# Optimization experiments

Hardware: AMD Instinct MI355X
Metric: run time of the kernel (lower is better)

Reference implementation:

```python
import jax, jax.numpy as jnp
import numpy as np

GRID = 2
SPAN = 2.0
EMBED = 64
HIDDEN = 128
PRED_LEN = 12
N = 1024
T = 8
SCENE_SIZE = 64


def _social_pool(ht, pos, scene, active):
    """ht: [N,H], pos: [N,2], scene: [N] int, active: [N] bool -> [N, GRID*GRID, H].
    Vectorized equivalent of the per-scene scatter_add pooling: pairwise mask over
    same-scene, active, within-area, non-self pairs; bin neighbor hidden states."""
    n = ht.shape[0]
    half = SPAN / 2.0
    eps = 0.01
    rel = pos[None, :, :] - pos[:, None, :]  # rel[i,j] = pos_j - pos_i
    within = ((rel[..., 0] < half - eps) & (rel[..., 0] > -half + eps)
              & (rel[..., 1] < half - eps) & (rel[..., 1] > -half + eps))
    pair = (within & (~jnp.eye(n, dtype=bool))
            & (scene[:, None] == scene[None, :])
            & active[:, None] & active[None, :])
    cell = SPAN / GRID
    gidx = jnp.floor((rel + half) / cell).astype(jnp.int32)
    gid = jnp.clip(gidx[..., 0] * GRID + gidx[..., 1], 0, GRID * GRID - 1)
    onehot = jax.nn.one_hot(gid, GRID * GRID, dtype=ht.dtype) * pair[..., None].astype(ht.dtype)
    # pooled[i,g,h] = sum_j onehot[i,j,g] * ht[j,h]
    return jnp.einsum('ijg,jh->igh', onehot, ht)


def _lstm_step(x, h, c, Wih, Whh, bih, bhh):
    z = x @ Wih.T + bih + h @ Whh.T + bhh
    i, f, g, o = jnp.split(z, 4, axis=-1)
    c_new = jax.nn.sigmoid(f) * c + jax.nn.sigmoid(i) * jnp.tanh(g)
    h_new = jax.nn.sigmoid(o) * jnp.tanh(c_new)
    return h_new, c_new


def setup_inputs() -> dict:
    key = jax.random.key(0)
    ks = jax.random.split(key, 16)
    past_traj = jax.random.uniform(ks[0], (N, T, 2), dtype=jnp.float32) * 8.0
    past_traj_rel = jax.random.normal(ks[1], (N, T, 2), dtype=jnp.float32)
    past_traj_timestamp_mask = jnp.ones((N, T), dtype=jnp.int32)
    is_predictable = jnp.ones((N, 1), dtype=jnp.int32)
    same_scene_mask = (jnp.arange(N, dtype=jnp.int32) // SCENE_SIZE).reshape(N, 1)

    def lin(k, fan_out, fan_in):
        b = 1.0 / np.sqrt(fan_in)
        return jax.random.uniform(k, (fan_out, fan_in), jnp.float32, -b, b)

    pos_W = lin(ks[2], EMBED, 2)
    pos_b = jnp.zeros((EMBED,), jnp.float32)
    soc_W = lin(ks[3], EMBED, GRID * GRID * HIDDEN)
    soc_b = jnp.zeros((EMBED,), jnp.float32)
    Wih = lin(ks[4], 4 * HIDDEN, 2 * EMBED)
    Whh = lin(ks[5], 4 * HIDDEN, HIDDEN)
    bih = jnp.zeros((4 * HIDDEN,), jnp.float32)
    bhh = jnp.zeros((4 * HIDDEN,), jnp.float32)
    h0 = jax.random.normal(ks[6], (HIDDEN,), jnp.float32) * 0.1
    c0 = jax.random.normal(ks[7], (HIDDEN,), jnp.float32) * 0.1
    pred_W = lin(ks[8], 5, HIDDEN)
    pred_b = jnp.zeros((5,), jnp.float32)
    return {
        'past_traj': past_traj, 'past_traj_rel': past_traj_rel,
        'past_traj_timestamp_mask': past_traj_timestamp_mask,
        'is_predictable': is_predictable, 'same_scene_mask': same_scene_mask,
        'pos_W': pos_W, 'pos_b': pos_b, 'soc_W': soc_W, 'soc_b': soc_b,
        'Wih': Wih, 'Whh': Whh, 'bih': bih, 'bhh': bhh,
        'h0': h0, 'c0': c0, 'pred_W': pred_W, 'pred_b': pred_b,
    }


def reference(past_traj, past_traj_rel, past_traj_timestamp_mask, is_predictable,
              same_scene_mask, pos_W, pos_b, soc_W, soc_b, Wih, Whh, bih, bhh,
              h0, c0, pred_W, pred_b):
    n = past_traj.shape[0]
    scene = same_scene_mask[:, 0]
    ht = jnp.broadcast_to(h0[None, :], (n, HIDDEN))
    ct = jnp.broadcast_to(c0[None, :], (n, HIDDEN))

    def obs_step(carry, inp):
        ht, ct = carry
        point, rel, m = inp  # [N,2], [N,2], [N]
        active = m == 1
        pooled = _social_pool(ht, point, scene, active)  # [N,G^2,H]
        et = jax.nn.relu(rel @ pos_W.T + pos_b)
        at = jax.nn.relu(pooled.reshape(n, -1) @ soc_W.T + soc_b)
        x = jnp.concatenate([et, at], axis=-1)
        h_new, c_new = _lstm_step(x, ht, ct, Wih, Whh, bih, bhh)
        ht = jnp.where(active[:, None], h_new, ht)
        ct = jnp.where(active[:, None], c_new, ct)
        return (ht, ct), None

    obs_inp = (jnp.moveaxis(past_traj, 1, 0), jnp.moveaxis(past_traj_rel, 1, 0),
               jnp.moveaxis(past_traj_timestamp_mask, 1, 0))
    (ht, ct), _ = jax.lax.scan(obs_step, (ht, ct), obs_inp)

    pred_active = past_traj_timestamp_mask[:, -1] == 1
    pos0 = past_traj[:, -1, :]

    def pred_step(carry, _):
        ht, ct, pos = carry
        out = ht @ pred_W.T + pred_b  # [N,5]
        rel = out[:, :2]
        pos = pos + rel
        pooled = _social_pool(ht, pos, scene, pred_active)
        et = jax.nn.relu(rel @ pos_W.T + pos_b)
        at = jax.nn.relu(pooled.reshape(n, -1) @ soc_W.T + soc_b)
        x = jnp.concatenate([et, at], axis=-1)
        h_new, c_new = _lstm_step(x, ht, ct, Wih, Whh, bih, bhh)
        ht = jnp.where(pred_active[:, None], h_new, ht)
        ct = jnp.where(pred_active[:, None], c_new, ct)
        return (ht, ct, pos), (out, pos)

    (_, _, _), (outs, trajs) = jax.lax.scan(pred_step, (ht, ct, pos0), None, length=PRED_LEN)
    pred_out_all = jnp.where(pred_active[:, None, None], jnp.moveaxis(outs, 0, 1), 0.0)
    pred_traj_all = jnp.where(pred_active[:, None, None], jnp.moveaxis(trajs, 0, 1), 0.0)
    # is_predictable is all-ones in this setup, so the final boolean filter is identity
    return pred_out_all, pred_traj_all
```

## Files before the change

### kernel.cpp

```cpp
#include <hip/hip_runtime.h>

#define NAGENT 64
#define HID    128
#define TOBS   8
#define PREDL  12
#define NTHR   1024
#define XH     136
#define PP     264
#define SPP    268

typedef __attribute__((ext_vector_type(8))) short bf16x8;
typedef __attribute__((ext_vector_type(4))) short bf16x4;
typedef __attribute__((ext_vector_type(4))) float f32x4;
typedef __attribute__((ext_vector_type(2))) unsigned int u32x2;

__device__ __forceinline__ unsigned short f2bf(float f) {
    unsigned int x = __float_as_uint(f);
    unsigned int r = (x + 0x7fffu + ((x >> 16) & 1u)) >> 16;
    return (unsigned short)r;
}
__device__ __forceinline__ float bf2f(unsigned short u) {
    return __uint_as_float(((unsigned int)u) << 16);
}
__device__ __forceinline__ float sigmf(float x) {
    return __builtin_amdgcn_rcpf(1.0f + __expf(-x));
}
__device__ __forceinline__ float tanhf_fast(float x) {
    x = fminf(fmaxf(x, -15.0f), 15.0f);
    float e = __expf(2.0f * x);
    return (e - 1.0f) * __builtin_amdgcn_rcpf(e + 1.0f);
}
__device__ __forceinline__ float sel4(float a0, float a1, float a2, float a3, int k) {
    float lo = (k & 1) ? a1 : a0;
    float hi = (k & 1) ? a3 : a2;
    return (k & 2) ? hi : lo;
}

__global__ void prep_weights(const float* __restrict__ Wih, const float* __restrict__ Whh,
                             const float* __restrict__ socW, const float* __restrict__ predW,
                             unsigned short* __restrict__ wd, unsigned short* __restrict__ wb,
                             unsigned short* __restrict__ wp) {
    int idx = blockIdx.x * 256 + threadIdx.x;
    if (idx < 131072) {
        int e = idx & 7, l = (idx >> 3) & 63, t = idx >> 9;
        int kt = t & 7, nt = t >> 3;
        int k = kt * 32 + ((l >> 4) << 3) + e;
        int n = nt * 16 + (l & 15);
        int d = n >> 2, g = n & 3;
        int row = g * 128 + d;
        float v = (k < 128) ? Wih[row * 128 + k] : Whh[row * 128 + (k - 128)];
        wd[idx] = f2bf(v);
    } else if (idx < 163840) {
        int i2 = idx - 131072;
        int e = i2 & 7, l = (i2 >> 3) & 63, t = i2 >> 9;
        int kt = t & 3, nt = t >> 2;
        int k = kt * 32 + ((l >> 4) << 3) + e;
        int r = nt * 16 + (l & 15);
        int eo = r >> 2, g = r & 3;
        wb[i2] = f2bf(socW[eo * 512 + g * 128 + k]);
    } else if (idx < 167936) {
        int i3 = idx - 163840;
        int e = i3 & 7, l = (i3 >> 3) & 63, f = i3 >> 9;
        int kt = f & 3, half = f >> 2;
        int k = kt * 32 + ((l >> 4) << 3) + e;
        int n = l & 15;
        float v = (n < 5) ? predW[n * 128 + k] : 0.0f;
        unsigned short hi = f2bf(v);
        wp[i3] = half ? f2bf(v - bf2f(hi)) : hi;
    }
}

__global__ __launch_bounds__(NTHR) void social_lstm_mfma(
    const float* __restrict__ past_traj, const float* __restrict__ past_traj_rel,
    const int* __restrict__ ts_mask, const int* __restrict__ scene_in,
    const float* __restrict__ pos_W, const float* __restrict__ pos_b,
    const float* __restrict__ soc_b,
    const float* __restrict__ bih, const float* __restrict__ bhh,
    const float* __restrict__ h0, const float* __restrict__ c0,
    const float* __restrict__ pred_b,
    const unsigned short* __restrict__ wd, const unsigned short* __restrict__ wb,
    const unsigned short* __restrict__ wp,
    float* __restrict__ out)
{
    __shared__ __align__(16) unsigned short sh_X[NAGENT][XH];
    __shared__ __align__(16) unsigned short sh_H[2][NAGENT][XH];
    __shared__ __align__(16) unsigned short sh_P[NAGENT][PP];
    __shared__ __align__(16) unsigned short sh_S[NAGENT][SPP];
    __shared__ float sh_px[2][NAGENT], sh_py[2][NAGENT];
    __shared__ float sh_rx[2][NAGENT], sh_ry[2][NAGENT];
    __shared__ __align__(16) int sh_act[2][NAGENT];
    __shared__ int sh_scene[NAGENT];

    const int tid  = threadIdx.x;
    const int lane = tid & 63;
    const int wv   = __builtin_amdgcn_readfirstlane(tid >> 6);
    const int gbase = blockIdx.x * NAGENT;
    const int c16 = lane & 15;
    const int q4  = lane >> 4;
    const int go  = c16 & 3;
    const int dq  = c16 >> 2;

    float bs[2], c_st[4][2], h_rg[4][2];
    int dimv[2];
    #pragma unroll
    for (int s = 0; s < 2; ++s) {
        const int n = (2 * wv + s) * 16 + c16;
        const int d = n >> 2, g = n & 3;
        bs[s] = bih[g * 128 + d] + bhh[g * 128 + d];
        dimv[s] = (2 * wv + s) * 4 + dq;
        const float hz = h0[dimv[s]], cz = c0[dimv[s]];
        #pragma unroll
        for (int mj = 0; mj < 4; ++mj) { c_st[mj][s] = cz; h_rg[mj][s] = hz; }
    }
    for (int p = tid; p < NAGENT * HID; p += NTHR) {
        int a = p >> 7, d = p & 127;
        sh_H[0][a][d] = f2bf(h0[d]);
    }
    if (tid < NAGENT) {
        const int ig = gbase + tid;
        sh_scene[tid] = scene_in[ig];
        sh_px[0][tid] = past_traj[(ig * TOBS + 0) * 2 + 0];
        sh_py[0][tid] = past_traj[(ig * TOBS + 0) * 2 + 1];
        sh_rx[0][tid] = past_traj_rel[(ig * TOBS + 0) * 2 + 0];
        sh_ry[0][tid] = past_traj_rel[(ig * TOBS + 0) * 2 + 1];
        sh_act[0][tid] = (ts_mask[ig * TOBS + 0] == 1) ? 1 : 0;
    }
    __syncthreads();

    const bf16x8* wdp = (const bf16x8*)wd + (2 * wv * 8) * 64 + lane;
    const bf16x8* wbv = (const bf16x8*)wb;

    for (int step = 0; step < TOBS + PREDL; ++step) {
        const int pb = step & 1;
        const int hb = step & 1;
        const int ab = (step < TOBS) ? pb : 1;

        if (step >= TOBS) {
            if (wv < 4) {
                const bf16x8* wpv = (const bf16x8*)wp;
                f32x4 pa = (f32x4){0.f, 0.f, 0.f, 0.f};
                #pragma unroll
                for (int kt = 0; kt < 4; ++kt) {
                    const bf16x8 a = *(const bf16x8*)&sh_H[hb][wv * 16 + c16][kt * 32 + q4 * 8];
                    pa = __builtin_amdgcn_mfma_f32_16x16x32_bf16(a, wpv[kt * 64 + lane], pa, 0, 0, 0);
                    pa = __builtin_amdgcn_mfma_f32_16x16x32_bf16(a, wpv[(4 + kt) * 64 + lane], pa, 0, 0, 0);
                }
                if (c16 < 5) {
                    const float pbias = pred_b[c16];
                    const int p = step - TOBS;
                    const int pprev = (step - 1) & 1;
                    #pragma unroll
                    for (int rr = 0; rr < 4; ++rr) {
                        const int a = wv * 16 + q4 * 4 + rr;
                        const float o = pa[rr] + pbias;
                        const float m = sh_act[1][a] ? 1.0f : 0.0f;
                        const int ig = gbase + a;
                        out[(ig * PREDL + p) * 5 + c16] = m * o;
                        if (c16 == 0) {
                            const float px = sh_px[pprev][a] + o;
                            sh_px[pb][a] = px; sh_rx[pb][a] = o;
                            out[61440 + (ig * PREDL + p) * 2 + 0] = m * px;
                        }
                        if (c16 == 1) {
                            const float py = sh_py[pprev][a] + o;
                            sh_py[pb][a] = py; sh_ry[pb][a] = o;
                            out[61440 + (ig * PREDL + p) * 2 + 1] = m * py;
                        }
                    }
                }
            } else {
                #pragma unroll
                for (int pass = 0; pass < 2; ++pass) {
                    const int tt = (pass == 0) ? (wv - 4) : (wv + 8);
                    if (pass == 1 && wv >= 8) break;
                    f32x4 acc2[4];
                    #pragma unroll
                    for (int mj = 0; mj < 4; ++mj) acc2[mj] = (f32x4){0.f, 0.f, 0.f, 0.f};
                    #pragma unroll
                    for (int kt = 0; kt < 4; ++kt) {
                        const bf16x8 b = wbv[(tt * 4 + kt) * 64 + lane];
                        #pragma unroll
                        for (int mj = 0; mj < 4; ++mj) {
                            const bf16x8 a = *(const bf16x8*)&sh_H[hb][mj * 16 + c16][kt * 32 + q4 * 8];
                            acc2[mj] = __builtin_amdgcn_mfma_f32_16x16x32_bf16(a, b, acc2[mj], 0, 0, 0);
                        }
                    }
                    const int rcol = tt * 16 + c16;
                    #pragma unroll
                    for (int mj = 0; mj < 4; ++mj)
                        #pragma unroll
                        for (int rr = 0; rr < 4; ++rr)
                            sh_S[mj * 16 + q4 * 4 + rr][rcol] = f2bf(acc2[mj][rr]);
                }
            }
            __syncthreads();
        }

        #pragma unroll
        for (int it = 0; it < 4; ++it) {
            const int p = it * NTHR + tid;
            const int i = p >> 6, j = p & 63;
            const float dx = sh_px[pb][j] - sh_px[pb][i];
            const float dy = sh_py[pb][j] - sh_py[pb][i];
            const bool within = (dx < 0.99f) & (dx > -0.99f) & (dy < 0.99f) & (dy > -0.99f);
            const bool pair = within && (i != j) && (sh_scene[i] == sh_scene[j])
                              && sh_act[ab][i] && sh_act[ab][j];
            const int gid = ((dx >= 0.f) ? 2 : 0) + ((dy >= 0.f) ? 1 : 0);
            unsigned int w0 = 0, w1 = 0;
            if (pair) {
                if (gid == 0) w0 = 0x3f80u;
                else if (gid == 1) w0 = 0x3f800000u;
                else if (gid == 2) w1 = 0x3f80u;
                else w1 = 0x3f800000u;
            }
            u32x2 w; w[0] = w0; w[1] = w1;
            *(u32x2*)&sh_P[i][j * 4] = w;
        }
        {
            const float rx = sh_rx[pb][lane], ry = sh_ry[pb][lane];
            const int e0 = wv * 4;
            #pragma unroll
            for (int u = 0; u < 4; ++u) {
                const int e = e0 + u;
                sh_X[lane][e] = f2bf(fmaxf(pos_b[e] + rx * pos_W[e * 2] + ry * pos_W[e * 2 + 1], 0.f));
            }
        }
        if (step < TOBS) {
            f32x4 acc2[4];
            #pragma unroll
            for (int mj = 0; mj < 4; ++mj) acc2[mj] = (f32x4){0.f, 0.f, 0.f, 0.f};
            #pragma unroll
            for (int kt = 0; kt < 4; ++kt) {
                const bf16x8 b = wbv[(wv * 4 + kt) * 64 + lane];
                #pragma unroll
                for (int mj = 0; mj < 4; ++mj) {
                    const bf16x8 a = *(const bf16x8*)&sh_H[hb][mj * 16 + c16][kt * 32 + q4 * 8];
                    acc2[mj] = __builtin_amdgcn_mfma_f32_16x16x32_bf16(a, b, acc2[mj], 0, 0, 0);
                }
            }
            const int rcol = wv * 16 + c16;
            #pragma unroll
            for (int mj = 0; mj < 4; ++mj)
                #pragma unroll
                for (int rr = 0; rr < 4; ++rr)
                    sh_S[mj * 16 + q4 * 4 + rr][rcol] = f2bf(acc2[mj][rr]);
        }
        __syncthreads();

        {
            const int mt = wv & 3, nt = wv >> 2;
            const int cb = 4 * (nt * 16 + c16);
            f32x4 cac = (f32x4){0.f, 0.f, 0.f, 0.f};
            #pragma unroll
            for (int kt = 0; kt < 8; ++kt) {
                const bf16x8 a = *(const bf16x8*)&sh_P[mt * 16 + c16][kt * 32 + q4 * 8];
                const int j0 = kt * 8 + q4 * 2;
                const bf16x4 lo = *(const bf16x4*)&sh_S[j0][cb];
                const bf16x4 hi = *(const bf16x4*)&sh_S[j0 + 1][cb];
                const bf16x8 b = __builtin_shufflevector(lo, hi, 0, 1, 2, 3, 4, 5, 6, 7);
                cac = __builtin_amdgcn_mfma_f32_16x16x32_bf16(a, b, cac, 0, 0, 0);
            }
            const int e = nt * 16 + c16;
            const float sb = soc_b[e];
            #pragma unroll
            for (int rr = 0; rr < 4; ++rr)
                sh_X[mt * 16 + q4 * 4 + rr][64 + e] = f2bf(fmaxf(cac[rr] + sb, 0.f));
        }
        __syncthreads();

        {
            f32x4 acc[4][2];
            #pragma unroll
            for (int mj = 0; mj < 4; ++mj) {
                acc[mj][0] = (f32x4){0.f, 0.f, 0.f, 0.f};
                acc[mj][1] = (f32x4){0.f, 0.f, 0.f, 0.f};
            }
            #pragma unroll 2
            for (int kt = 0; kt < 8; ++kt) {
                const bf16x8 b0 = wdp[kt * 64];
                const bf16x8 b1 = wdp[kt * 64 + 512];
                #pragma unroll
                for (int mj = 0; mj < 4; ++mj) {
                    const bf16x8 a = (kt < 4)
                        ? *(const bf16x8*)&sh_X[mj * 16 + c16][kt * 32 + q4 * 8]
                        : *(const bf16x8*)&sh_H[hb][mj * 16 + c16][(kt - 4) * 32 + q4 * 8];
                    acc[mj][0] = __builtin_amdgcn_mfma_f32_16x16x32_bf16(a, b0, acc[mj][0], 0, 0, 0);
                    acc[mj][1] = __builtin_amdgcn_mfma_f32_16x16x32_bf16(a, b1, acc[mj][1], 0, 0, 0);
                }
            }
            #pragma unroll
            for (int mj = 0; mj < 4; ++mj) {
                const int a = mj * 16 + q4 * 4 + go;
                const bool act = sh_act[ab][a] != 0;
                #pragma unroll
                for (int s = 0; s < 2; ++s) {
                    const float z0 = acc[mj][s][0] + bs[s];
                    const float z1 = acc[mj][s][1] + bs[s];
                    const float z2 = acc[mj][s][2] + bs[s];
                    const float z3 = acc[mj][s][3] + bs[s];
                    const float s0 = sel4(z0, z1, z2, z3, go);
                    const float s1 = sel4(z0, z1, z2, z3, go ^ 1);
                    const float s2 = sel4(z0, z1, z2, z3, go ^ 2);
                    const float s3 = sel4(z0, z1, z2, z3, go ^ 3);
                    const float t1 = __shfl_xor(s1, 1, 64);
                    const float t2 = __shfl_xor(s2, 2, 64);
                    const float t3 = __shfl_xor(s3, 3, 64);
                    const float zi = sel4(s0, t1, t2, t3, go);
                    const float zf = sel4(s0, t1, t2, t3, go ^ 1);
                    const float zg = sel4(s0, t1, t2, t3, go ^ 2);
                    const float zo = sel4(s0, t1, t2, t3, go ^ 3);
                    const float cold = c_st[mj][s];
                    const float cn = sigmf(zf) * cold + sigmf(zi) * tanhf_fast(zg);
                    const float hn = sigmf(zo) * tanhf_fast(cn);
                    c_st[mj][s] = act ? cn : cold;
                    h_rg[mj][s] = act ? hn : h_rg[mj][s];
                    sh_H[hb ^ 1][a][dimv[s]] = f2bf(h_rg[mj][s]);
                }
            }
        }
        if (step + 1 < TOBS && tid < NAGENT) {
            const int ig = gbase + tid;
            const int np = (step + 1) & 1;
            sh_px[np][tid] = past_traj[(ig * TOBS + step + 1) * 2 + 0];
            sh_py[np][tid] = past_traj[(ig * TOBS + step + 1) * 2 + 1];
            sh_rx[np][tid] = past_traj_rel[(ig * TOBS + step + 1) * 2 + 0];
            sh_ry[np][tid] = past_traj_rel[(ig * TOBS + step + 1) * 2 + 1];
            sh_act[np][tid] = (ts_mask[ig * TOBS + step + 1] == 1) ? 1 : 0;
        }
        __syncthreads();
    }
}

extern "C" void kernel_launch(void* const* d_in, const int* in_sizes, int n_in,
                              void* d_out, int out_size, void* d_ws, size_t ws_size,
                              hipStream_t stream) {
    (void)in_sizes; (void)n_in; (void)out_size; (void)ws_size;
    unsigned short* wd = (unsigned short*)d_ws;
    unsigned short* wb = wd + 131072;
    unsigned short* wp = wb + 32768;
    prep_weights<<<656, 256, 0, stream>>>(
        (const float*)d_in[9], (const float*)d_in[10],
        (const float*)d_in[7], (const float*)d_in[15], wd, wb, wp);
    social_lstm_mfma<<<16, NTHR, 0, stream>>>(
        (const float*)d_in[0],
        (const float*)d_in[1],
        (const int*)  d_in[2],
        (const int*)  d_in[4],
        (const float*)d_in[5],
        (const float*)d_in[6],
        (const float*)d_in[8],
        (const float*)d_in[11],
        (const float*)d_in[12],
        (const float*)d_in[13],
        (const float*)d_in[14],
        (const float*)d_in[16],
        wd, wb, wp,
        (float*)d_out);
}
```

Before: 287.8 us.

## Hoist recurrent h@Whh MFMAs before barrier and use cheaper activation math

The recurrent half of the LSTM gate GEMM (h @ Whh, which reads only the previous hidden state) now runs in the social-pooling phase before the barrier, overlapping it with pooling work. Only the input half (sh_X) is accumulated after the barrier, which shortens the critical path per timestep. Sigmoid and tanh now use exp2 with a single reciprocal, and tanh drops its clamp. The bf16 conversion now uses the HIP intrinsic, and the pooling mask word is built with a branchless shift. Keeping the accumulators live across the barrier adds register pressure, which could hurt occupancy or cause spills.

After: 344.5 us. 1.2x slower.

```diff
diff --git a/kernel.cpp b/kernel.cpp
--- a/kernel.cpp
+++ b/kernel.cpp
@@ -1,4 +1,5 @@
 #include <hip/hip_runtime.h>
+#include <hip/hip_bf16.h>
 
 #define NAGENT 64
 #define HID    128
@@ -15,20 +16,18 @@
 typedef __attribute__((ext_vector_type(2))) unsigned int u32x2;
 
 __device__ __forceinline__ unsigned short f2bf(float f) {
-    unsigned int x = __float_as_uint(f);
-    unsigned int r = (x + 0x7fffu + ((x >> 16) & 1u)) >> 16;
-    return (unsigned short)r;
+    __hip_bfloat16 h = __float2bfloat16(f);
+    return __builtin_bit_cast(unsigned short, h);
 }
 __device__ __forceinline__ float bf2f(unsigned short u) {
     return __uint_as_float(((unsigned int)u) << 16);
 }
 __device__ __forceinline__ float sigmf(float x) {
-    return __builtin_amdgcn_rcpf(1.0f + __expf(-x));
+    return __builtin_amdgcn_rcpf(1.0f + __builtin_amdgcn_exp2f(x * -1.442695041f));
 }
 __device__ __forceinline__ float tanhf_fast(float x) {
-    x = fminf(fmaxf(x, -15.0f), 15.0f);
-    float e = __expf(2.0f * x);
-    return (e - 1.0f) * __builtin_amdgcn_rcpf(e + 1.0f);
+    const float s = __builtin_amdgcn_rcpf(1.0f + __builtin_amdgcn_exp2f(x * -2.885390082f));
+    return __builtin_fmaf(2.0f, s, -1.0f);
 }
 __device__ __forceinline__ float sel4(float a0, float a1, float a2, float a3, int k) {
     float lo = (k & 1) ? a1 : a0;
@@ -206,15 +205,9 @@
             const bool pair = within && (i != j) && (sh_scene[i] == sh_scene[j])
                               && sh_act[ab][i] && sh_act[ab][j];
             const int gid = ((dx >= 0.f) ? 2 : 0) + ((dy >= 0.f) ? 1 : 0);
-            unsigned int w0 = 0, w1 = 0;
-            if (pair) {
-                if (gid == 0) w0 = 0x3f80u;
-                else if (gid == 1) w0 = 0x3f800000u;
-                else if (gid == 2) w1 = 0x3f80u;
-                else w1 = 0x3f800000u;
-            }
-            u32x2 w; w[0] = w0; w[1] = w1;
-            *(u32x2*)&sh_P[i][j * 4] = w;
+            const unsigned long long w = pair ? (0x3f80ull << (gid << 4)) : 0ull;
+            u32x2 wv2; wv2[0] = (unsigned int)w; wv2[1] = (unsigned int)(w >> 32);
+            *(u32x2*)&sh_P[i][j * 4] = wv2;
         }
         {
             const float rx = sh_rx[pb][lane], ry = sh_ry[pb][lane];
@@ -247,6 +240,12 @@
         }
         __syncthreads();
 
+        f32x4 acc[4][2];
+        #pragma unroll
+        for (int mj = 0; mj < 4; ++mj) {
+            acc[mj][0] = (f32x4){0.f, 0.f, 0.f, 0.f};
+            acc[mj][1] = (f32x4){0.f, 0.f, 0.f, 0.f};
+        }
         {
             const int mt = wv & 3, nt = wv >> 2;
             const int cb = 4 * (nt * 16 + c16);
@@ -266,24 +265,27 @@
             for (int rr = 0; rr < 4; ++rr)
                 sh_X[mt * 16 + q4 * 4 + rr][64 + e] = f2bf(fmaxf(cac[rr] + sb, 0.f));
         }
+        #pragma unroll
+        for (int kt = 4; kt < 8; ++kt) {
+            const bf16x8 b0 = wdp[kt * 64];
+            const bf16x8 b1 = wdp[kt * 64 + 512];
+            #pragma unroll
+            for (int mj = 0; mj < 4; ++mj) {
+                const bf16x8 a = *(const bf16x8*)&sh_H[hb][mj * 16 + c16][(kt - 4) * 32 + q4 * 8];
+                acc[mj][0] = __builtin_amdgcn_mfma_f32_16x16x32_bf16(a, b0, acc[mj][0], 0, 0, 0);
+                acc[mj][1] = __builtin_amdgcn_mfma_f32_16x16x32_bf16(a, b1, acc[mj][1], 0, 0, 0);
+            }
+        }
         __syncthreads();
 
         {
-            f32x4 acc[4][2];
-            #pragma unroll
-            for (int mj = 0; mj < 4; ++mj) {
-                acc[mj][0] = (f32x4){0.f, 0.f, 0.f, 0.f};
-                acc[mj][1] = (f32x4){0.f, 0.f, 0.f, 0.f};
-            }
-            #pragma unroll 2
-            for (int kt = 0; kt < 8; ++kt) {
+            #pragma unroll
+            for (int kt = 0; kt < 4; ++kt) {
                 const bf16x8 b0 = wdp[kt * 64];
                 const bf16x8 b1 = wdp[kt * 64 + 512];
                 #pragma unroll
                 for (int mj = 0; mj < 4; ++mj) {
-                    const bf16x8 a = (kt < 4)
-                        ? *(const bf16x8*)&sh_X[mj * 16 + c16][kt * 32 + q4 * 8]
-                        : *(const bf16x8*)&sh_H[hb][mj * 16 + c16][(kt - 4) * 32 + q4 * 8];
+                    const bf16x8 a = *(const bf16x8*)&sh_X[mj * 16 + c16][kt * 32 + q4 * 8];
                     acc[mj][0] = __builtin_amdgcn_mfma_f32_16x16x32_bf16(a, b0, acc[mj][0], 0, 0, 0);
                     acc[mj][1] = __builtin_amdgcn_mfma_f32_16x16x32_bf16(a, b1, acc[mj][1], 0, 0, 0);
                 }
```
